# Kernel tuning notes

Hardware: AMD Instinct MI355X
Metric: run time of the kernel (lower is better)

## Reference

```python
import jax, jax.numpy as jnp
import numpy as np

B, N, D_IN, D_HID = 8, 2048, 5, 32

def setup_inputs() -> dict:
    key = jax.random.key(0)
    k1, k2, k3, k4 = jax.random.split(key, 4)
    s = jax.random.normal(k1, (B, N, D_IN), dtype=jnp.float32)
    Gmat = jax.random.uniform(k2, (B, N, N), dtype=jnp.float32)
    Qweight = jax.random.normal(k3, (D_IN, D_HID), dtype=jnp.float32)
    Kweight = jax.random.normal(k4, (D_IN, D_HID), dtype=jnp.float32)
    return {"s": s, "Gmat": Gmat, "Qweight": Qweight, "Kweight": Kweight}

def reference(s, Gmat, Qweight, Kweight):
    # s: [B, N, 5]; Gmat: [B, N, N] (or [N, N], broadcastable)
    if Gmat.ndim == 2:
        Gmat = Gmat[None]
    q = jnp.einsum('bnd,dm->bnm', s, Qweight)   # [B, N, 32]
    k = jnp.einsum('bnd,dm->bnm', s, Kweight)   # [B, N, 32]
    att = jnp.square(jnp.einsum('bnm,bjm->bnj', q, k)) * Gmat  # [B, N, N]
    att = att / (jnp.sum(att, axis=2, keepdims=True) + 0.001)
    return att
```

## Files before the change

### kernel.cpp

```cpp
#include <hip/hip_runtime.h>

constexpr int Bc   = 8;
constexpr int Nc   = 2048;
constexpr int DIN  = 5;
constexpr int DHID = 32;

__global__ __launch_bounds__(256) void u_precompute(
    const float* __restrict__ s, const float* __restrict__ Qw,
    const float* __restrict__ Kw, float* __restrict__ u)
{
    __shared__ float Msh[DIN * DIN];
    const int tid = threadIdx.x;
    if (tid < DIN * DIN) {
        const int d = tid / DIN, e = tid % DIN;
        float acc = 0.f;
        #pragma unroll
        for (int m = 0; m < DHID; ++m)
            acc = fmaf(Qw[d * DHID + m], Kw[e * DHID + m], acc);
        Msh[tid] = acc;
    }
    __syncthreads();
    const int g = blockIdx.x * 256 + tid;
    if (g >= Bc * Nc) return;
    const int b = g >> 11;
    const int j = g & (Nc - 1);
    float sv[DIN];
    #pragma unroll
    for (int e = 0; e < DIN; ++e) sv[e] = s[(size_t)g * DIN + e];
    #pragma unroll
    for (int d = 0; d < DIN; ++d) {
        float acc = 0.f;
        #pragma unroll
        for (int e = 0; e < DIN; ++e) acc = fmaf(Msh[d * DIN + e], sv[e], acc);
        u[((size_t)b * DIN + d) * Nc + j] = acc;
    }
}

__global__ __launch_bounds__(256) void att_row_u(
    const float* __restrict__ s, const float* __restrict__ G,
    const float* __restrict__ u, float* __restrict__ out, long gbs)
{
    const int row = blockIdx.x;
    const int b   = row >> 11;
    const int i   = row & (Nc - 1);
    const int tid = threadIdx.x;

    float si[DIN];
    #pragma unroll
    for (int d = 0; d < DIN; ++d) si[d] = s[(size_t)row * DIN + d];

    const float* gRow = G + (size_t)b * gbs + (size_t)i * Nc;
    const float* ub   = u + (size_t)b * DIN * Nc;
    float*       oRow = out + (size_t)row * Nc;

    float a[2][4];
    float lsum = 0.f;
    #pragma unroll
    for (int it = 0; it < 2; ++it) {
        const int j0 = it * 1024 + tid * 4;
        const float4 g4 = *reinterpret_cast<const float4*>(gRow + j0);
        float vx = 0.f, vy = 0.f, vz = 0.f, vw = 0.f;
        #pragma unroll
        for (int d = 0; d < DIN; ++d) {
            const float4 ud = *reinterpret_cast<const float4*>(ub + (size_t)d * Nc + j0);
            vx = fmaf(si[d], ud.x, vx);
            vy = fmaf(si[d], ud.y, vy);
            vz = fmaf(si[d], ud.z, vz);
            vw = fmaf(si[d], ud.w, vw);
        }
        a[it][0] = vx * vx * g4.x;
        a[it][1] = vy * vy * g4.y;
        a[it][2] = vz * vz * g4.z;
        a[it][3] = vw * vw * g4.w;
        lsum += (a[it][0] + a[it][1]) + (a[it][2] + a[it][3]);
    }

    #pragma unroll
    for (int off = 32; off > 0; off >>= 1)
        lsum += __shfl_xor(lsum, off, 64);
    __shared__ float wpart[4];
    if ((tid & 63) == 0) wpart[tid >> 6] = lsum;
    __syncthreads();
    const float total = (wpart[0] + wpart[1]) + (wpart[2] + wpart[3]);
    const float inv = 1.0f / (total + 0.001f);

    #pragma unroll
    for (int it = 0; it < 2; ++it) {
        const int j0 = it * 1024 + tid * 4;
        float4 o;
        o.x = a[it][0] * inv;
        o.y = a[it][1] * inv;
        o.z = a[it][2] * inv;
        o.w = a[it][3] * inv;
        *reinterpret_cast<float4*>(oRow + j0) = o;
    }
}

__global__ __launch_bounds__(256) void att_row_direct(
    const float* __restrict__ s, const float* __restrict__ G,
    const float* __restrict__ Qw, const float* __restrict__ Kw,
    float* __restrict__ out, long gbs)
{
    __shared__ float Msh[DIN * DIN];
    __shared__ float wpart[4];
    const int tid = threadIdx.x;
    if (tid < DIN * DIN) {
        const int d = tid / DIN, e = tid % DIN;
        float acc = 0.f;
        #pragma unroll
        for (int m = 0; m < DHID; ++m)
            acc = fmaf(Qw[d * DHID + m], Kw[e * DHID + m], acc);
        Msh[tid] = acc;
    }
    __syncthreads();

    const int row = blockIdx.x;
    const int b   = row >> 11;
    const int i   = row & (Nc - 1);

    float w[DIN];
    {
        float si[DIN];
        #pragma unroll
        for (int e = 0; e < DIN; ++e) si[e] = s[(size_t)row * DIN + e];
        #pragma unroll
        for (int d = 0; d < DIN; ++d) {
            float acc = 0.f;
            #pragma unroll
            for (int e = 0; e < DIN; ++e) acc = fmaf(si[e], Msh[e * DIN + d], acc);
            w[d] = acc;
        }
    }

    const float* gRow = G + (size_t)b * gbs + (size_t)i * Nc;
    const float* sb   = s + (size_t)b * Nc * DIN;
    float*       oRow = out + (size_t)row * Nc;

    float a[2][4];
    float lsum = 0.f;
    #pragma unroll
    for (int it = 0; it < 2; ++it) {
        const int j0 = it * 1024 + tid * 4;
        const float4 g4 = *reinterpret_cast<const float4*>(gRow + j0);
        float v[4];
        #pragma unroll
        for (int c = 0; c < 4; ++c) {
            const float* sj = sb + (size_t)(j0 + c) * DIN;
            float acc = 0.f;
            #pragma unroll
            for (int d = 0; d < DIN; ++d) acc = fmaf(w[d], sj[d], acc);
            v[c] = acc;
        }
        a[it][0] = v[0] * v[0] * g4.x;
        a[it][1] = v[1] * v[1] * g4.y;
        a[it][2] = v[2] * v[2] * g4.z;
        a[it][3] = v[3] * v[3] * g4.w;
        lsum += (a[it][0] + a[it][1]) + (a[it][2] + a[it][3]);
    }

    #pragma unroll
    for (int off = 32; off > 0; off >>= 1)
        lsum += __shfl_xor(lsum, off, 64);
    if ((tid & 63) == 0) wpart[tid >> 6] = lsum;
    __syncthreads();
    const float total = (wpart[0] + wpart[1]) + (wpart[2] + wpart[3]);
    const float inv = 1.0f / (total + 0.001f);

    #pragma unroll
    for (int it = 0; it < 2; ++it) {
        const int j0 = it * 1024 + tid * 4;
        float4 o;
        o.x = a[it][0] * inv;
        o.y = a[it][1] * inv;
        o.z = a[it][2] * inv;
        o.w = a[it][3] * inv;
        *reinterpret_cast<float4*>(oRow + j0) = o;
    }
}

extern "C" void kernel_launch(void* const* d_in, const int* in_sizes, int n_in,
                              void* d_out, int out_size, void* d_ws, size_t ws_size,
                              hipStream_t stream)
{
    const float* s  = (const float*)d_in[0];
    const float* G  = (const float*)d_in[1];
    const float* Qw = (const float*)d_in[2];
    const float* Kw = (const float*)d_in[3];
    float* out = (float*)d_out;

    const long gbs = (in_sizes[1] == Nc * Nc) ? 0L : (long)Nc * Nc;

    const size_t uBytes = (size_t)Bc * DIN * Nc * sizeof(float);
    if (ws_size >= uBytes) {
        float* u = (float*)d_ws;
        u_precompute<<<(Bc * Nc + 255) / 256, 256, 0, stream>>>(s, Qw, Kw, u);
        att_row_u<<<Bc * Nc, 256, 0, stream>>>(s, G, u, out, gbs);
    } else {
        att_row_direct<<<Bc * Nc, 256, 0, stream>>>(s, G, Qw, Kw, out, gbs);
    }
}
```

Baseline: 251.9 us.

## Map one wavefront per row and use nontemporal output stores

New measurement: 251.6 us. About the same (-0.1%).

```diff
diff --git a/kernel.cpp b/kernel.cpp
--- a/kernel.cpp
+++ b/kernel.cpp
@@ -4,6 +4,8 @@
 constexpr int Nc   = 2048;
 constexpr int DIN  = 5;
 constexpr int DHID = 32;
+
+typedef float vf4 __attribute__((ext_vector_type(4)));
 
 __global__ __launch_bounds__(256) void u_precompute(
     const float* __restrict__ s, const float* __restrict__ Qw,
@@ -36,63 +38,65 @@
     }
 }
 
-__global__ __launch_bounds__(256) void att_row_u(
+__global__ __launch_bounds__(256) void att_wave_row(
     const float* __restrict__ s, const float* __restrict__ G,
     const float* __restrict__ u, float* __restrict__ out, long gbs)
 {
-    const int row = blockIdx.x;
-    const int b   = row >> 11;
-    const int i   = row & (Nc - 1);
-    const int tid = threadIdx.x;
-
-    float si[DIN];
-    #pragma unroll
-    for (int d = 0; d < DIN; ++d) si[d] = s[(size_t)row * DIN + d];
+    const int tid  = threadIdx.x;
+    const int lane = tid & 63;
+    const int wid  = tid >> 6;
+    const int row  = blockIdx.x * 4 + wid;
+    const int b    = row >> 11;
+    const int i    = row & (Nc - 1);
 
     const float* gRow = G + (size_t)b * gbs + (size_t)i * Nc;
     const float* ub   = u + (size_t)b * DIN * Nc;
     float*       oRow = out + (size_t)row * Nc;
 
-    float a[2][4];
-    float lsum = 0.f;
-    #pragma unroll
-    for (int it = 0; it < 2; ++it) {
-        const int j0 = it * 1024 + tid * 4;
-        const float4 g4 = *reinterpret_cast<const float4*>(gRow + j0);
+    float si[DIN];
+    #pragma unroll
+    for (int d = 0; d < DIN; ++d) si[d] = s[(size_t)row * DIN + d];
+
+    float4 g4[8];
+    #pragma unroll
+    for (int k = 0; k < 8; ++k)
+        g4[k] = *reinterpret_cast<const float4*>(gRow + k * 256 + lane * 4);
+
+    float a[8][4];
+    float psum = 0.f;
+    #pragma unroll
+    for (int k = 0; k < 8; ++k) {
+        const int j0 = k * 256 + lane * 4;
         float vx = 0.f, vy = 0.f, vz = 0.f, vw = 0.f;
         #pragma unroll
         for (int d = 0; d < DIN; ++d) {
-            const float4 ud = *reinterpret_cast<const float4*>(ub + (size_t)d * Nc + j0);
-            vx = fmaf(si[d], ud.x, vx);
-            vy = fmaf(si[d], ud.y, vy);
-            vz = fmaf(si[d], ud.z, vz);
-            vw = fmaf(si[d], ud.w, vw);
+            const float4 u4 = *reinterpret_cast<const float4*>(ub + (size_t)d * Nc + j0);
+            vx = fmaf(si[d], u4.x, vx);
+            vy = fmaf(si[d], u4.y, vy);
+            vz = fmaf(si[d], u4.z, vz);
+            vw = fmaf(si[d], u4.w, vw);
         }
-        a[it][0] = vx * vx * g4.x;
-        a[it][1] = vy * vy * g4.y;
-        a[it][2] = vz * vz * g4.z;
-        a[it][3] = vw * vw * g4.w;
-        lsum += (a[it][0] + a[it][1]) + (a[it][2] + a[it][3]);
+        a[k][0] = vx * vx * g4[k].x;
+        a[k][1] = vy * vy * g4[k].y;
+        a[k][2] = vz * vz * g4[k].z;
+        a[k][3] = vw * vw * g4[k].w;
+        psum += (a[k][0] + a[k][1]) + (a[k][2] + a[k][3]);
     }
 
     #pragma unroll
     for (int off = 32; off > 0; off >>= 1)
-        lsum += __shfl_xor(lsum, off, 64);
-    __shared__ float wpart[4];
-    if ((tid & 63) == 0) wpart[tid >> 6] = lsum;
-    __syncthreads();
-    const float total = (wpart[0] + wpart[1]) + (wpart[2] + wpart[3]);
-    const float inv = 1.0f / (total + 0.001f);
-
-    #pragma unroll
-    for (int it = 0; it < 2; ++it) {
-        const int j0 = it * 1024 + tid * 4;
-        float4 o;
-        o.x = a[it][0] * inv;
-        o.y = a[it][1] * inv;
-        o.z = a[it][2] * inv;
-        o.w = a[it][3] * inv;
-        *reinterpret_cast<float4*>(oRow + j0) = o;
+        psum += __shfl_xor(psum, off, 64);
+    const float inv = 1.0f / (psum + 0.001f);
+
+    #pragma unroll
+    for (int k = 0; k < 8; ++k) {
+        const int j0 = k * 256 + lane * 4;
+        vf4 o;
+        o.x = a[k][0] * inv;
+        o.y = a[k][1] * inv;
+        o.z = a[k][2] * inv;
+        o.w = a[k][3] * inv;
+        __builtin_nontemporal_store(o, reinterpret_cast<vf4*>(oRow + j0));
     }
 }
 
@@ -169,12 +173,12 @@
     #pragma unroll
     for (int it = 0; it < 2; ++it) {
         const int j0 = it * 1024 + tid * 4;
-        float4 o;
+        vf4 o;
         o.x = a[it][0] * inv;
         o.y = a[it][1] * inv;
         o.z = a[it][2] * inv;
         o.w = a[it][3] * inv;
-        *reinterpret_cast<float4*>(oRow + j0) = o;
+        __builtin_nontemporal_store(o, reinterpret_cast<vf4*>(oRow + j0));
     }
 }
 
@@ -194,7 +198,7 @@
     if (ws_size >= uBytes) {
         float* u = (float*)d_ws;
         u_precompute<<<(Bc * Nc + 255) / 256, 256, 0, stream>>>(s, Qw, Kw, u);
-        att_row_u<<<Bc * Nc, 256, 0, stream>>>(s, G, u, out, gbs);
+        att_wave_row<<<(Bc * Nc) / 4, 256, 0, stream>>>(s, G, u, out, gbs);
     } else {
         att_row_direct<<<Bc * Nc, 256, 0, stream>>>(s, G, Qw, Kw, out, gbs);
     }
```
